# Kernel optimization log

Measured on AMD Instinct MI355X. Metric: run time of the kernel, lower is better.

Reference implementation:

```python
import jax, jax.numpy as jnp
import numpy as np

C, PH, PW, H, W = 10, 7, 7, 34, 34
STRIDE = 8.0
S = 4  # sample_per_part


def setup_inputs() -> dict:
    key = jax.random.key(0)
    k1, k2, k3, k4, k5 = jax.random.split(key, 5)
    N = 30000
    ft = jax.random.normal(k1, (1, C * PH * PW, H, W), dtype=jnp.float32)
    x1 = jax.random.uniform(k2, (N,), dtype=jnp.float32) * 200.0
    y1 = jax.random.uniform(k3, (N,), dtype=jnp.float32) * 200.0
    bw = jax.random.uniform(k4, (N,), dtype=jnp.float32) * 70.0 + 2.0
    bh = jax.random.uniform(k5, (N,), dtype=jnp.float32) * 70.0 + 2.0
    rois = jnp.stack([jnp.zeros((N,), jnp.float32), x1, y1, x1 + bw, y1 + bh], axis=1)
    return {"ft_add_left_right": ft, "rois": rois}


def reference(ft_add_left_right, rois):
    ft = ft_add_left_right[0].reshape(C, PH, PW, H, W)
    roi_start_w = rois[:, 1] / STRIDE
    roi_start_h = rois[:, 2] / STRIDE
    roi_end_w = rois[:, 3] / STRIDE
    roi_end_h = rois[:, 4] / STRIDE
    # torch.threshold(x, 0.1, 0.1): x if x > 0.1 else 0.1
    roi_height = jnp.where(roi_end_h - roi_start_h > 0.1, roi_end_h - roi_start_h, 0.1)
    roi_width = jnp.where(roi_end_w - roi_start_w > 0.1, roi_end_w - roi_start_w, 0.1)
    bin_size_h = roi_height / PH
    bin_size_w = roi_width / PW
    sub_h = bin_size_h / S
    sub_w = bin_size_w / S

    gh, gw = jnp.meshgrid(jnp.arange(PH), jnp.arange(PW), indexing='ij')
    phs = gh.reshape(-1, 1)  # [49,1]
    pws = gw.reshape(-1, 1)  # [49,1]
    hstart = jnp.floor(roi_start_h + phs * bin_size_h)  # [49,N]
    wstart = jnp.floor(roi_start_w + pws * bin_size_w)  # [49,N]

    N = rois.shape[0]
    sum_ = jnp.zeros((C, PH * PW, N), jnp.float32)
    count = jnp.zeros((PH * PW, N), jnp.float32)

    for ih in range(S):
        for iw in range(S):
            w = wstart + (iw + 0.5) * sub_w  # [49,N]
            h = hstart + (ih + 0.5) * sub_h
            keep = (w > -1) & (w < W) & (h > -1) & (h < H)
            x1 = jnp.floor(w).astype(jnp.int32)
            x2 = jnp.ceil(w).astype(jnp.int32)
            y1 = jnp.floor(h).astype(jnp.int32)
            y2 = jnp.ceil(h).astype(jnp.int32)
            x1v = (x1 >= 0) & (x1 < W)
            x2v = (x2 >= 0) & (x2 < W)
            y1v = (y1 >= 0) & (y1 < H)
            y2v = (y2 >= 0) & (y2 < H)
            x1 = jnp.clip(x1, 0, W - 1)
            x2 = jnp.clip(x2, 0, W - 1)
            y1 = jnp.clip(y1, 0, H - 1)
            y2 = jnp.clip(y2, 0, H - 1)
            dist_x = w - x1
            dist_y = h - y1
            # gathers: result [C,49,N]
            v11 = ft[:, phs, pws, y1, x1]
            v12 = ft[:, phs, pws, y2, x1]
            v21 = ft[:, phs, pws, y1, x2]
            v22 = ft[:, phs, pws, y2, x2]
            # faithful to source: ALL four masks zero value11 only (source bug)
            bad11 = (~x1v & y1v) | (~x1v & y2v) | (~x2v & y1v) | (~x2v & y2v)
            v11 = jnp.where(bad11, 0.0, v11)
            value = ((1 - dist_x) * (1 - dist_y) * v11
                     + (1 - dist_x) * dist_y * v12
                     + dist_x * (1 - dist_y) * v21
                     + dist_x * dist_y * v22)
            sum_ = sum_ + jnp.where(keep, value, 0.0)
            count = count + keep.astype(jnp.float32)

    out = jnp.where(count > 0, sum_ / jnp.maximum(count, 1.0), sum_)
    return jnp.transpose(out, (2, 0, 1))  # [N, C, 49]
```

## Files before the change

### kernel.cpp

```cpp
#include <hip/hip_runtime.h>


#define NC 10
#define NBIN 49
#define FH 34
#define FW 34
#define PLANE (FH * FW)
#define CSTRIDE 16
#define RPB 16
#define TSTRIDE 491
#define NSIDE 14

__global__ __launch_bounds__(256) void prep_kernel(
    const float* __restrict__ ft, float* __restrict__ ftT)
{
    const int p = blockIdx.x * 256 + threadIdx.x;
    if (p >= NBIN * PLANE) return;
    float v[NC];
#pragma unroll
    for (int c = 0; c < NC; ++c) v[c] = ft[c * (NBIN * PLANE) + p];
    float4* d = reinterpret_cast<float4*>(ftT + (size_t)p * CSTRIDE);
    d[0] = make_float4(v[0], v[1], v[2], v[3]);
    d[1] = make_float4(v[4], v[5], v[6], v[7]);
    d[2] = make_float4(v[8], v[9], 0.f, 0.f);
}

__global__ __launch_bounds__(256) void main_kernel(
    const float* __restrict__ rois, const float* __restrict__ ftT,
    const float* __restrict__ ft, float* __restrict__ out, int N, int use_t)
{
    __shared__ float sides[NSIDE][RPB][8];
    __shared__ float tile[RPB][TSTRIDE];

    const int r = threadIdx.x & (RPB - 1);
    const int s = threadIdx.x >> 4;
    const int n = blockIdx.x * RPB + r;
    const bool valid = (n < N);

    float rsw = 0.f, rsh = 0.f, rew = 0.f, reh = 0.f;
    if (valid) {
        rsw = rois[n * 5 + 1] * 0.125f;
        rsh = rois[n * 5 + 2] * 0.125f;
        rew = rois[n * 5 + 3] * 0.125f;
        reh = rois[n * 5 + 4] * 0.125f;
    }
    float rheight = __fsub_rn(reh, rsh);
    if (!(rheight > 0.1f)) rheight = 0.1f;
    float rwidth = __fsub_rn(rew, rsw);
    if (!(rwidth > 0.1f)) rwidth = 0.1f;
    const float bsh   = __fdiv_rn(rheight, 7.0f);
    const float bsw   = __fdiv_rn(rwidth, 7.0f);
    const float sub_h = __fdiv_rn(bsh, 4.0f);
    const float sub_w = __fdiv_rn(bsw, 4.0f);

    if (s < NSIDE) {
        const bool isY = (s < 7);
        const int  k   = isY ? s : s - 7;
        const float st = isY ? rsh : rsw;
        const float bs = isY ? bsh : bsw;
        const float sb = isY ? sub_h : sub_w;
        const float start = floorf(__fadd_rn(st, __fmul_rn((float)k, bs)));

        float A[3] = {0.f, 0.f, 0.f}, B[3] = {0.f, 0.f, 0.f};
        float cnt = 0.f;
        int P0 = 0;
#pragma unroll
        for (int i = 0; i < 4; ++i) {
            const float h = __fadd_rn(start, __fmul_rn((float)i + 0.5f, sb));
            const bool ok = (h > -1.0f) && (h < 34.0f);
            const int p1 = (int)floorf(h);
            const int p2 = (int)ceilf(h);
            const bool v1 = (p1 >= 0) && (p1 < 34);
            const bool v2 = (p2 >= 0) && (p2 < 34);
            const int p1c = min(max(p1, 0), 33);
            const int p2c = min(max(p2, 0), 33);
            const float d = __fsub_rn(h, (float)p1c);
            if (i == 0) P0 = p1c;
            const int i1 = p1c - P0, i2 = p2c - P0;
            const float t1 = ok ? (1.0f - d) : 0.0f;
            const float t2 = ok ? d : 0.0f;
            const bool bsel = isY ? (v1 || v2) : ((!v1) || (!v2));
            const float tb = (ok && bsel) ? (1.0f - d) : 0.0f;
            cnt += ok ? 1.0f : 0.0f;
#pragma unroll
            for (int p = 0; p < 3; ++p) {
                A[p] += (i1 == p) ? t1 : 0.0f;
                A[p] += (i2 == p) ? t2 : 0.0f;
                B[p] += (i1 == p) ? tb : 0.0f;
            }
        }
        float* sp = &sides[s][r][0];
        sp[0] = A[0]; sp[1] = A[1]; sp[2] = A[2];
        sp[3] = B[0]; sp[4] = B[1]; sp[5] = B[2];
        sp[6] = cnt;  sp[7] = (float)P0;
    }
    __syncthreads();

#pragma unroll
    for (int j = 0; j < 4; ++j) {
        const int bin = j * RPB + s;
        if (valid && bin < NBIN) {
            const int ph = bin / 7;
            const int pw = bin - ph * 7;

            const float4 ya = *(const float4*)&sides[ph][r][0];
            const float4 yb = *(const float4*)&sides[ph][r][4];
            const float4 xa = *(const float4*)&sides[7 + pw][r][0];
            const float4 xb = *(const float4*)&sides[7 + pw][r][4];
            const float AY[3] = {ya.x, ya.y, ya.z};
            const float BY[3] = {ya.w, yb.x, yb.y};
            const float cntY  = yb.z;
            const int   Y0    = (int)yb.w;
            const float AX[3] = {xa.x, xa.y, xa.z};
            const float BX[3] = {xa.w, xb.x, xb.y};
            const float cntX  = xb.z;
            const int   X0    = (int)xb.w;

            const int binbase = bin * PLANE;
            const int rowo[3] = {binbase + Y0 * FW,
                                 binbase + min(Y0 + 1, FH - 1) * FW,
                                 binbase + min(Y0 + 2, FH - 1) * FW};
            const int colo[3] = {X0, min(X0 + 1, FW - 1), min(X0 + 2, FW - 1)};

            float wgt[9];
            int   off[9];
#pragma unroll
            for (int p = 0; p < 3; ++p)
#pragma unroll
                for (int q = 0; q < 3; ++q) {
                    const float w = AY[p] * AX[q] - BY[p] * BX[q];
                    wgt[3 * p + q] = w;
                    off[3 * p + q] = (w != 0.0f) ? (rowo[p] + colo[q]) : binbase;
                }

            float sum[NC];
#pragma unroll
            for (int c = 0; c < NC; ++c) sum[c] = 0.f;

            if (use_t) {
#pragma unroll
                for (int k = 0; k < 9; ++k) {
                    const float* pix = ftT + (size_t)off[k] * CSTRIDE;
                    const float4 a  = *(const float4*)pix;
                    const float4 b  = *(const float4*)(pix + 4);
                    const float2 c2 = *(const float2*)(pix + 8);
                    const float w = wgt[k];
                    sum[0] = fmaf(w, a.x, sum[0]);
                    sum[1] = fmaf(w, a.y, sum[1]);
                    sum[2] = fmaf(w, a.z, sum[2]);
                    sum[3] = fmaf(w, a.w, sum[3]);
                    sum[4] = fmaf(w, b.x, sum[4]);
                    sum[5] = fmaf(w, b.y, sum[5]);
                    sum[6] = fmaf(w, b.z, sum[6]);
                    sum[7] = fmaf(w, b.w, sum[7]);
                    sum[8] = fmaf(w, c2.x, sum[8]);
                    sum[9] = fmaf(w, c2.y, sum[9]);
                }
            } else {
#pragma unroll
                for (int k = 0; k < 9; ++k) {
                    const float w = wgt[k];
#pragma unroll
                    for (int c = 0; c < NC; ++c)
                        sum[c] = fmaf(w, ft[c * (NBIN * PLANE) + off[k]], sum[c]);
                }
            }

            const float cnt = cntY * cntX;
            const float inv = (cnt > 0.0f) ? __fdiv_rn(1.0f, cnt) : 1.0f;
            float* tp = &tile[r][0];
#pragma unroll
            for (int c = 0; c < NC; ++c) tp[c * NBIN + bin] = sum[c] * inv;
        }
    }

    __syncthreads();

    const int n0 = blockIdx.x * RPB;
    for (int i = threadIdx.x; i < RPB * (NC * NBIN); i += 256) {
        const int row = i / (NC * NBIN);
        const int col = i - row * (NC * NBIN);
        const int n2 = n0 + row;
        if (n2 < N) out[(size_t)n2 * (NC * NBIN) + col] = tile[row][col];
    }
}

extern "C" void kernel_launch(void* const* d_in, const int* in_sizes, int n_in,
                              void* d_out, int out_size, void* d_ws, size_t ws_size,
                              hipStream_t stream) {
    const float* ft   = (const float*)d_in[0];
    const float* rois = (const float*)d_in[1];
    float* out        = (float*)d_out;
    const int N = in_sizes[1] / 5;

    const size_t need = (size_t)NBIN * PLANE * CSTRIDE * sizeof(float);
    const int use_t = (ws_size >= need) ? 1 : 0;
    float* ftT = (float*)d_ws;

    if (use_t) {
        const int npix = NBIN * PLANE;
        prep_kernel<<<(npix + 255) / 256, 256, 0, stream>>>(ft, ftT);
    }
    main_kernel<<<(N + RPB - 1) / RPB, 256, 0, stream>>>(rois, ftT, ft, out, N, use_t);
}
```

Before: 125.8 us.

## Map one thread per (roi, bin) and drop shared-memory staging

Replaces the block-of-16-ROIs scheme, which precomputed side weights in shared memory and staged the output tile through LDS, with a flat one-thread-per-(roi,bin) mapping. Each thread recomputes its own Y and X side weights and writes its 10 channel outputs directly to global memory with stride 49. This removes the two __syncthreads, the shared-memory use and the cooperative copy-out, and it improves occupancy. The cost is redundant side computation per bin and strided, partially coalesced output stores (adjacent threads write adjacent bins).

```diff
diff --git a/kernel.cpp b/kernel.cpp
--- a/kernel.cpp
+++ b/kernel.cpp
@@ -7,9 +7,6 @@
 #define FW 34
 #define PLANE (FH * FW)
 #define CSTRIDE 16
-#define RPB 16
-#define TSTRIDE 491
-#define NSIDE 14
 
 __global__ __launch_bounds__(256) void prep_kernel(
     const float* __restrict__ ft, float* __restrict__ ftT)
@@ -25,25 +22,54 @@
     d[2] = make_float4(v[8], v[9], 0.f, 0.f);
 }
 
+__device__ __forceinline__ void side_compute(
+    float st, float bs, float sb, int k, bool isY,
+    float A[3], float B[3], float& cnt, int& P0)
+{
+    const float start = floorf(__fadd_rn(st, __fmul_rn((float)k, bs)));
+#pragma unroll
+    for (int i = 0; i < 4; ++i) {
+        const float h = __fadd_rn(start, __fmul_rn((float)i + 0.5f, sb));
+        const bool ok = (h > -1.0f) && (h < 34.0f);
+        const int p1 = (int)floorf(h);
+        const int p2 = (int)ceilf(h);
+        const bool v1 = (p1 >= 0) && (p1 < 34);
+        const bool v2 = (p2 >= 0) && (p2 < 34);
+        const int p1c = min(max(p1, 0), 33);
+        const int p2c = min(max(p2, 0), 33);
+        const float d = __fsub_rn(h, (float)p1c);
+        if (i == 0) P0 = p1c;
+        const int i1 = p1c - P0, i2 = p2c - P0;
+        const float t1 = ok ? (1.0f - d) : 0.0f;
+        const float t2 = ok ? d : 0.0f;
+        const bool bsel = isY ? (v1 || v2) : ((!v1) || (!v2));
+        const float tb = (ok && bsel) ? (1.0f - d) : 0.0f;
+        cnt += ok ? 1.0f : 0.0f;
+#pragma unroll
+        for (int p = 0; p < 3; ++p) {
+            A[p] += (i1 == p) ? t1 : 0.0f;
+            A[p] += (i2 == p) ? t2 : 0.0f;
+            B[p] += (i1 == p) ? tb : 0.0f;
+        }
+    }
+}
+
 __global__ __launch_bounds__(256) void main_kernel(
     const float* __restrict__ rois, const float* __restrict__ ftT,
     const float* __restrict__ ft, float* __restrict__ out, int N, int use_t)
 {
-    __shared__ float sides[NSIDE][RPB][8];
-    __shared__ float tile[RPB][TSTRIDE];
+    const int i = blockIdx.x * 256 + threadIdx.x;
+    if (i >= N * NBIN) return;
+    const int n   = i / NBIN;
+    const int bin = i - n * NBIN;
+    const int ph  = bin / 7;
+    const int pw  = bin - ph * 7;
 
-    const int r = threadIdx.x & (RPB - 1);
-    const int s = threadIdx.x >> 4;
-    const int n = blockIdx.x * RPB + r;
-    const bool valid = (n < N);
+    const float rsw = rois[n * 5 + 1] * 0.125f;
+    const float rsh = rois[n * 5 + 2] * 0.125f;
+    const float rew = rois[n * 5 + 3] * 0.125f;
+    const float reh = rois[n * 5 + 4] * 0.125f;
 
-    float rsw = 0.f, rsh = 0.f, rew = 0.f, reh = 0.f;
-    if (valid) {
-        rsw = rois[n * 5 + 1] * 0.125f;
-        rsh = rois[n * 5 + 2] * 0.125f;
-        rew = rois[n * 5 + 3] * 0.125f;
-        reh = rois[n * 5 + 4] * 0.125f;
-    }
     float rheight = __fsub_rn(reh, rsh);
     if (!(rheight > 0.1f)) rheight = 0.1f;
     float rwidth = __fsub_rn(rew, rsw);
@@ -53,136 +79,69 @@
     const float sub_h = __fdiv_rn(bsh, 4.0f);
     const float sub_w = __fdiv_rn(bsw, 4.0f);
 
-    if (s < NSIDE) {
-        const bool isY = (s < 7);
-        const int  k   = isY ? s : s - 7;
-        const float st = isY ? rsh : rsw;
-        const float bs = isY ? bsh : bsw;
-        const float sb = isY ? sub_h : sub_w;
-        const float start = floorf(__fadd_rn(st, __fmul_rn((float)k, bs)));
+    float AY[3] = {0.f, 0.f, 0.f}, BY[3] = {0.f, 0.f, 0.f};
+    float AX[3] = {0.f, 0.f, 0.f}, BX[3] = {0.f, 0.f, 0.f};
+    float cntY = 0.f, cntX = 0.f;
+    int Y0 = 0, X0 = 0;
+    side_compute(rsh, bsh, sub_h, ph, true,  AY, BY, cntY, Y0);
+    side_compute(rsw, bsw, sub_w, pw, false, AX, BX, cntX, X0);
 
-        float A[3] = {0.f, 0.f, 0.f}, B[3] = {0.f, 0.f, 0.f};
-        float cnt = 0.f;
-        int P0 = 0;
+    const int binbase = bin * PLANE;
+    const int rowo[3] = {binbase + Y0 * FW,
+                         binbase + min(Y0 + 1, FH - 1) * FW,
+                         binbase + min(Y0 + 2, FH - 1) * FW};
+    const int colo[3] = {X0, min(X0 + 1, FW - 1), min(X0 + 2, FW - 1)};
+
+    float wgt[9];
+    int   off[9];
 #pragma unroll
-        for (int i = 0; i < 4; ++i) {
-            const float h = __fadd_rn(start, __fmul_rn((float)i + 0.5f, sb));
-            const bool ok = (h > -1.0f) && (h < 34.0f);
-            const int p1 = (int)floorf(h);
-            const int p2 = (int)ceilf(h);
-            const bool v1 = (p1 >= 0) && (p1 < 34);
-            const bool v2 = (p2 >= 0) && (p2 < 34);
-            const int p1c = min(max(p1, 0), 33);
-            const int p2c = min(max(p2, 0), 33);
-            const float d = __fsub_rn(h, (float)p1c);
-            if (i == 0) P0 = p1c;
-            const int i1 = p1c - P0, i2 = p2c - P0;
-            const float t1 = ok ? (1.0f - d) : 0.0f;
-            const float t2 = ok ? d : 0.0f;
-            const bool bsel = isY ? (v1 || v2) : ((!v1) || (!v2));
-            const float tb = (ok && bsel) ? (1.0f - d) : 0.0f;
-            cnt += ok ? 1.0f : 0.0f;
+    for (int p = 0; p < 3; ++p)
 #pragma unroll
-            for (int p = 0; p < 3; ++p) {
-                A[p] += (i1 == p) ? t1 : 0.0f;
-                A[p] += (i2 == p) ? t2 : 0.0f;
-                B[p] += (i1 == p) ? tb : 0.0f;
-            }
+        for (int q = 0; q < 3; ++q) {
+            const float w = AY[p] * AX[q] - BY[p] * BX[q];
+            wgt[3 * p + q] = w;
+            off[3 * p + q] = (w != 0.0f) ? (rowo[p] + colo[q]) : binbase;
         }
-        float* sp = &sides[s][r][0];
-        sp[0] = A[0]; sp[1] = A[1]; sp[2] = A[2];
-        sp[3] = B[0]; sp[4] = B[1]; sp[5] = B[2];
-        sp[6] = cnt;  sp[7] = (float)P0;
-    }
-    __syncthreads();
 
+    float sum[NC];
 #pragma unroll
-    for (int j = 0; j < 4; ++j) {
-        const int bin = j * RPB + s;
-        if (valid && bin < NBIN) {
-            const int ph = bin / 7;
-            const int pw = bin - ph * 7;
+    for (int c = 0; c < NC; ++c) sum[c] = 0.f;
 
-            const float4 ya = *(const float4*)&sides[ph][r][0];
-            const float4 yb = *(const float4*)&sides[ph][r][4];
-            const float4 xa = *(const float4*)&sides[7 + pw][r][0];
-            const float4 xb = *(const float4*)&sides[7 + pw][r][4];
-            const float AY[3] = {ya.x, ya.y, ya.z};
-            const float BY[3] = {ya.w, yb.x, yb.y};
-            const float cntY  = yb.z;
-            const int   Y0    = (int)yb.w;
-            const float AX[3] = {xa.x, xa.y, xa.z};
-            const float BX[3] = {xa.w, xb.x, xb.y};
-            const float cntX  = xb.z;
-            const int   X0    = (int)xb.w;
-
-            const int binbase = bin * PLANE;
-            const int rowo[3] = {binbase + Y0 * FW,
-                                 binbase + min(Y0 + 1, FH - 1) * FW,
-                                 binbase + min(Y0 + 2, FH - 1) * FW};
-            const int colo[3] = {X0, min(X0 + 1, FW - 1), min(X0 + 2, FW - 1)};
-
-            float wgt[9];
-            int   off[9];
+    if (use_t) {
 #pragma unroll
-            for (int p = 0; p < 3; ++p)
+        for (int k = 0; k < 9; ++k) {
+            const float* pix = ftT + (size_t)off[k] * CSTRIDE;
+            const float4 a  = *(const float4*)pix;
+            const float4 b  = *(const float4*)(pix + 4);
+            const float2 c2 = *(const float2*)(pix + 8);
+            const float w = wgt[k];
+            sum[0] = fmaf(w, a.x, sum[0]);
+            sum[1] = fmaf(w, a.y, sum[1]);
+            sum[2] = fmaf(w, a.z, sum[2]);
+            sum[3] = fmaf(w, a.w, sum[3]);
+            sum[4] = fmaf(w, b.x, sum[4]);
+            sum[5] = fmaf(w, b.y, sum[5]);
+            sum[6] = fmaf(w, b.z, sum[6]);
+            sum[7] = fmaf(w, b.w, sum[7]);
+            sum[8] = fmaf(w, c2.x, sum[8]);
+            sum[9] = fmaf(w, c2.y, sum[9]);
+        }
+    } else {
 #pragma unroll
-                for (int q = 0; q < 3; ++q) {
-                    const float w = AY[p] * AX[q] - BY[p] * BX[q];
-                    wgt[3 * p + q] = w;
-                    off[3 * p + q] = (w != 0.0f) ? (rowo[p] + colo[q]) : binbase;
-                }
-
-            float sum[NC];
+        for (int k = 0; k < 9; ++k) {
+            const float w = wgt[k];
 #pragma unroll
-            for (int c = 0; c < NC; ++c) sum[c] = 0.f;
-
-            if (use_t) {
-#pragma unroll
-                for (int k = 0; k < 9; ++k) {
-                    const float* pix = ftT + (size_t)off[k] * CSTRIDE;
-                    const float4 a  = *(const float4*)pix;
-                    const float4 b  = *(const float4*)(pix + 4);
-                    const float2 c2 = *(const float2*)(pix + 8);
-                    const float w = wgt[k];
-                    sum[0] = fmaf(w, a.x, sum[0]);
-                    sum[1] = fmaf(w, a.y, sum[1]);
-                    sum[2] = fmaf(w, a.z, sum[2]);
-                    sum[3] = fmaf(w, a.w, sum[3]);
-                    sum[4] = fmaf(w, b.x, sum[4]);
-                    sum[5] = fmaf(w, b.y, sum[5]);
-                    sum[6] = fmaf(w, b.z, sum[6]);
-                    sum[7] = fmaf(w, b.w, sum[7]);
-                    sum[8] = fmaf(w, c2.x, sum[8]);
-                    sum[9] = fmaf(w, c2.y, sum[9]);
-                }
-            } else {
-#pragma unroll
-                for (int k = 0; k < 9; ++k) {
-                    const float w = wgt[k];
-#pragma unroll
-                    for (int c = 0; c < NC; ++c)
-                        sum[c] = fmaf(w, ft[c * (NBIN * PLANE) + off[k]], sum[c]);
-                }
-            }
-
-            const float cnt = cntY * cntX;
-            const float inv = (cnt > 0.0f) ? __fdiv_rn(1.0f, cnt) : 1.0f;
-            float* tp = &tile[r][0];
-#pragma unroll
-            for (int c = 0; c < NC; ++c) tp[c * NBIN + bin] = sum[c] * inv;
+            for (int c = 0; c < NC; ++c)
+                sum[c] = fmaf(w, ft[c * (NBIN * PLANE) + off[k]], sum[c]);
         }
     }
 
-    __syncthreads();
+    const float cnt = cntY * cntX;
+    const float inv = (cnt > 0.0f) ? __fdiv_rn(1.0f, cnt) : 1.0f;
 
-    const int n0 = blockIdx.x * RPB;
-    for (int i = threadIdx.x; i < RPB * (NC * NBIN); i += 256) {
-        const int row = i / (NC * NBIN);
-        const int col = i - row * (NC * NBIN);
-        const int n2 = n0 + row;
-        if (n2 < N) out[(size_t)n2 * (NC * NBIN) + col] = tile[row][col];
-    }
+    float* op = out + (size_t)n * (NC * NBIN) + bin;
+#pragma unroll
+    for (int c = 0; c < NC; ++c) op[c * NBIN] = sum[c] * inv;
 }
 
 extern "C" void kernel_launch(void* const* d_in, const int* in_sizes, int n_in,
@@ -201,5 +160,6 @@
         const int npix = NBIN * PLANE;
         prep_kernel<<<(npix + 255) / 256, 256, 0, stream>>>(ft, ftT);
     }
-    main_kernel<<<(N + RPB - 1) / RPB, 256, 0, stream>>>(rois, ftT, ft, out, N, use_t);
+    const long long total = (long long)N * NBIN;
+    main_kernel<<<(int)((total + 255) / 256), 256, 0, stream>>>(rois, ftT, ft, out, N, use_t);
 }
```

Result: slower. 149.9 us (+19.2%).
